# Optimization experiments

Measured on AMD Instinct MI355X. Metric: run time of the kernel, lower is better.

## Reference

```python
import jax, jax.numpy as jnp
import numpy as np

BN_EPS = 1e-5


def grid_sample_bilinear(img, grid):
    """Torch F.grid_sample, mode=bilinear, padding_mode=zeros, align_corners=False.
    img: (B, C, H, W); grid: (B, N, 2) in [-1, 1] -> (B, C, N)."""
    B, C, H, W = img.shape
    x = ((grid[..., 0] + 1.0) * W - 1.0) * 0.5  # (B, N) pixel coords
    y = ((grid[..., 1] + 1.0) * H - 1.0) * 0.5
    x0 = jnp.floor(x)
    y0 = jnp.floor(y)
    x1 = x0 + 1.0
    y1 = y0 + 1.0
    wx1 = x - x0
    wx0 = 1.0 - wx1
    wy1 = y - y0
    wy0 = 1.0 - wy1
    img_flat = img.reshape(B, C, H * W)

    def corner(xi, yi, w):
        valid = (xi >= 0) & (xi <= W - 1) & (yi >= 0) & (yi <= H - 1)
        xi_c = jnp.clip(xi, 0, W - 1).astype(jnp.int32)
        yi_c = jnp.clip(yi, 0, H - 1).astype(jnp.int32)
        idx = yi_c * W + xi_c  # (B, N)
        vals = jnp.take_along_axis(img_flat, idx[:, None, :], axis=2)  # (B, C, N)
        return vals * (w * valid.astype(img.dtype))[:, None, :]

    return (corner(x0, y0, wx0 * wy0) + corner(x1, y0, wx1 * wy0)
            + corner(x0, y1, wx0 * wy1) + corner(x1, y1, wx1 * wy1))


def conv1x1(x, w, b):
    # x: (B, Cin, N), w: (Cout, Cin), b: (Cout,)
    return jnp.einsum('oi,bin->bon', w, x) + b[None, :, None]


def batchnorm1d_train(x, gamma, beta):
    # training-mode BN over (batch, length) per channel, biased variance
    mean = jnp.mean(x, axis=(0, 2), keepdims=True)
    var = jnp.mean((x - mean) ** 2, axis=(0, 2), keepdims=True)
    xn = (x - mean) * jax.lax.rsqrt(var + BN_EPS)
    return xn * gamma[None, :, None] + beta[None, :, None]


def setup_inputs() -> dict:
    key = jax.random.key(0)
    ks = jax.random.split(key, 12)
    B, N, CI, CP, H, W, R = 4, 16384, 256, 256, 64, 160, 4
    Cin = CI + CP
    Cb = CP // R

    def glorot(k, shape):
        fan_in = shape[1]
        return jax.random.normal(k, shape, dtype=jnp.float32) * (1.0 / np.sqrt(fan_in))

    return {
        'pts_img': jax.random.uniform(ks[0], (B, N, 2), dtype=jnp.float32, minval=-1.0, maxval=1.0),
        'img_feats': jax.random.normal(ks[1], (B, CI, H, W), dtype=jnp.float32),
        'pts_feats': jax.random.normal(ks[2], (B, CP, N), dtype=jnp.float32),
        'fusion_w': glorot(ks[3], (CP, Cin)),
        'fusion_b': jax.random.normal(ks[4], (CP,), dtype=jnp.float32) * 0.01,
        'bn_gamma': jnp.ones((CP,), dtype=jnp.float32),
        'bn_beta': jnp.zeros((CP,), dtype=jnp.float32),
        'ca1_w': glorot(ks[5], (Cb, CP)),
        'ca1_b': jax.random.normal(ks[6], (Cb,), dtype=jnp.float32) * 0.01,
        'ca2_w': glorot(ks[7], (CP, Cb)),
        'ca2_b': jax.random.normal(ks[8], (CP,), dtype=jnp.float32) * 0.01,
        'sa_w': glorot(ks[9], (Cb, CP)),
        'sa_b': jax.random.normal(ks[10], (Cb,), dtype=jnp.float32) * 0.01,
    }


def reference(pts_img, img_feats, pts_feats, fusion_w, fusion_b, bn_gamma, bn_beta,
              ca1_w, ca1_b, ca2_w, ca2_b, sa_w, sa_b):
    # grid_sample gather: (B, C_I, N)
    pts_wise_img_feats = grid_sample_bilinear(img_feats, pts_img)
    fusion = jnp.concatenate([pts_wise_img_feats, pts_feats], axis=1)  # (B, C_I+C_P, N)
    # fusion MLP: conv1x1 + BN + ReLU
    fusion = jax.nn.relu(batchnorm1d_train(conv1x1(fusion, fusion_w, fusion_b), bn_gamma, bn_beta))
    # spatial attention: max over channels of bottleneck conv, sigmoid gate
    spatial = jax.nn.sigmoid(jnp.max(conv1x1(fusion, sa_w, sa_b), axis=1, keepdims=True))
    fusion = spatial * fusion
    # channel attention: bottleneck MLP, global max-pool over points, sigmoid gate
    ca = conv1x1(jax.nn.relu(conv1x1(fusion, ca1_w, ca1_b)), ca2_w, ca2_b)  # (B, C_P, N)
    channel = jax.nn.sigmoid(jnp.max(ca, axis=2, keepdims=True))  # (B, C_P, 1)
    return channel * fusion
```

## Files before the change

### kernel.cpp

```cpp
#include <hip/hip_runtime.h>
#include <stdint.h>


typedef __attribute__((ext_vector_type(8))) short bf16x8;
typedef __attribute__((ext_vector_type(4))) float f32x4;

#define B_ 4
#define N_ 16384
#define H_ 64
#define W_ 160
#define HW_ (H_ * W_)
#define K_ 512

__device__ __forceinline__ float bf2f(unsigned short u) {
    union { unsigned int i; float f; } c; c.i = ((unsigned int)u) << 16; return c.f;
}
__device__ __forceinline__ unsigned short f2bf(float f) {
    union { float f; unsigned int i; } c; c.f = f;
    unsigned int u = c.i;
    return (unsigned short)((u + 0x7FFFu + ((u >> 16) & 1u)) >> 16);
}
__device__ __forceinline__ unsigned int fkey(float f) {
    union { float f; unsigned int u; int i; } c; c.f = f;
    return (c.i < 0) ? ~c.u : (c.u | 0x80000000u);
}
__device__ __forceinline__ float funkey(unsigned int k) {
    union { unsigned int u; float f; } c;
    c.u = (k & 0x80000000u) ? (k & 0x7FFFFFFFu) : ~k;
    return c.f;
}

__device__ __forceinline__ void async_copy16(void* lds, const void* g) {
#if defined(__has_builtin) && __has_builtin(__builtin_amdgcn_global_load_lds)
    __builtin_amdgcn_global_load_lds(
        (const __attribute__((address_space(1))) unsigned int*)g,
        (__attribute__((address_space(3))) unsigned int*)lds, 16, 0, 0);
#else
    *(uint4*)lds = *(const uint4*)g;
#endif
}

__global__ __launch_bounds__(256) void k_imgt(const float* __restrict__ img,
                                              unsigned short* __restrict__ imgT,
                                              const float* __restrict__ fw,
                                              const float* __restrict__ saw,
                                              const float* __restrict__ c1w,
                                              const float* __restrict__ c2w,
                                              unsigned short* WfB, unsigned short* saB,
                                              unsigned short* ca1B, unsigned short* ca2B,
                                              float* buckets, unsigned int* camax) {
    int t = threadIdx.x;
    int bx = blockIdx.x;
    if (bx < 2560) {
        __shared__ __align__(16) unsigned short tile[64 * 68];
        int hw0 = (bx % 160) * 64, c0 = ((bx / 160) & 3) * 64, b = bx / 640;
        const float* src = img + ((size_t)b * 256 + c0) * HW_ + hw0;
        int sub = (t & 15) * 4, grp = t >> 4;
#pragma unroll
        for (int it = 0; it < 4; ++it) {
            int cl = grp + it * 16;
            float4 v = *(const float4*)(src + (size_t)cl * HW_ + sub);
            ushort4 o;
            o.x = f2bf(v.x); o.y = f2bf(v.y); o.z = f2bf(v.z); o.w = f2bf(v.w);
            *(ushort4*)(tile + cl * 68 + sub) = o;
        }
        __syncthreads();
        unsigned short* dst = imgT + ((size_t)b * HW_ + hw0) * 256 + c0;
#pragma unroll
        for (int it = 0; it < 4; ++it) {
            int hwl = grp + it * 16;
            ushort4 o;
            o.x = tile[(sub + 0) * 68 + hwl];
            o.y = tile[(sub + 1) * 68 + hwl];
            o.z = tile[(sub + 2) * 68 + hwl];
            o.w = tile[(sub + 3) * 68 + hwl];
            *(ushort4*)(dst + (size_t)hwl * 256 + sub) = o;
        }
    } else {
        int j = bx - 2560;
        if (j == 0) {
            for (int i = t; i < 16 * 512; i += 256) buckets[i] = 0.f;
            for (int i = t; i < 8 * 1024; i += 256) camax[i] = 0u;
        }
        int i = j * 256 + t;
        if (i < 131072) WfB[i] = f2bf(fw[i]);
        else if (i < 147456) saB[i - 131072] = f2bf(saw[i - 131072]);
        else if (i < 163840) ca1B[i - 147456] = f2bf(c1w[i - 147456]);
        else if (i < 180224) ca2B[i - 163840] = f2bf(c2w[i - 163840]);
    }
}

__global__ __launch_bounds__(256, 2) void k_gemm1f(const unsigned short* __restrict__ WfB,
                                                   const float* __restrict__ pim,
                                                   const unsigned short* __restrict__ imgT,
                                                   const float* __restrict__ pts,
                                                   const float* __restrict__ fb,
                                                   unsigned short* __restrict__ Y,
                                                   float* __restrict__ buckets) {
    __shared__ __align__(16) char smem[37888];
    unsigned short* At = (unsigned short*)smem;
    unsigned short* Bt = (unsigned short*)(smem + 16384);
    uint4*  offs4 = (uint4*)(smem + 26624);
    float4* wts4  = (float4*)(smem + 28672);
    unsigned short* tile = (unsigned short*)smem;
    float* biasS = (float*)(smem + 34816);
    float* redS  = (float*)(smem + 35840);
    float* redQ  = (float*)(smem + 36864);

    int t = threadIdx.x;
    int n0 = blockIdx.x * 128, bb = blockIdx.y;
    int w = t >> 6, lane = t & 63, quad = lane >> 4, l15 = lane & 15;
    const unsigned short* imb = imgT + (size_t)bb * HW_ * 256;

    if (t < 128) {
        float2 g2 = *(const float2*)(pim + (size_t)((size_t)bb * N_ + n0 + t) * 2);
        float x = (g2.x + 1.0f) * (0.5f * W_) - 0.5f;
        float y = (g2.y + 1.0f) * (0.5f * H_) - 0.5f;
        float xf = floorf(x), yf = floorf(y);
        float wx1 = x - xf, wx0 = 1.0f - wx1;
        float wy1 = y - yf, wy0 = 1.0f - wy1;
        int x0 = (int)xf, y0 = (int)yf;
        int x1 = x0 + 1, y1 = y0 + 1;
        float vx0 = (x0 >= 0 && x0 < W_) ? 1.f : 0.f;
        float vx1 = (x1 >= 0 && x1 < W_) ? 1.f : 0.f;
        float vy0 = (y0 >= 0 && y0 < H_) ? 1.f : 0.f;
        float vy1 = (y1 >= 0 && y1 < H_) ? 1.f : 0.f;
        int cx0 = min(max(x0, 0), W_ - 1), cx1 = min(max(x1, 0), W_ - 1);
        int cy0 = min(max(y0, 0), H_ - 1), cy1 = min(max(y1, 0), H_ - 1);
        uint4 o4;
        o4.x = (unsigned)(cy0 * W_ + cx0);
        o4.y = (unsigned)(cy0 * W_ + cx1);
        o4.z = (unsigned)(cy1 * W_ + cx0);
        o4.w = (unsigned)(cy1 * W_ + cx1);
        offs4[t] = o4;
        float4 w4;
        w4.x = wx0 * wy0 * vx0 * vy0;
        w4.y = wx1 * wy0 * vx1 * vy0;
        w4.z = wx0 * wy1 * vx0 * vy1;
        w4.w = wx1 * wy1 * vx1 * vy1;
        wts4[t] = w4;
    }

    const f32x4 fzero = {0.f, 0.f, 0.f, 0.f};
    f32x4 acc[4][8];
#pragma unroll
    for (int i = 0; i < 4; ++i)
#pragma unroll
        for (int j = 0; j < 8; ++j) acc[i][j] = fzero;

    for (int kt = 0; kt < 16; ++kt) {
        int k0 = kt * 32;
        __syncthreads();
#pragma unroll
        for (int q = 0; q < 4; ++q) {
            int row = q * 64 + (t >> 2);
            async_copy16(At + (size_t)q * 2048 + (size_t)t * 8,
                         WfB + (size_t)row * K_ + k0 + (t & 3) * 8);
        }
        if (kt < 8) {
#pragma unroll
            for (int pass = 0; pass < 2; ++pass) {
                int tau = pass * 256 + t;
                int pt = tau >> 2, cg = tau & 3;
                uint4 o4 = offs4[pt];
                float4 w4 = wts4[pt];
                int ch = k0 + cg * 8;
                uint4 cA = *(const uint4*)(imb + (size_t)o4.x * 256 + ch);
                uint4 cB = *(const uint4*)(imb + (size_t)o4.y * 256 + ch);
                uint4 cC = *(const uint4*)(imb + (size_t)o4.z * 256 + ch);
                uint4 cD = *(const uint4*)(imb + (size_t)o4.w * 256 + ch);
                const unsigned short* pa = (const unsigned short*)&cA;
                const unsigned short* pb = (const unsigned short*)&cB;
                const unsigned short* pc = (const unsigned short*)&cC;
                const unsigned short* pd = (const unsigned short*)&cD;
                uint4 ov;
                unsigned short* po = (unsigned short*)&ov;
#pragma unroll
                for (int e = 0; e < 8; ++e)
                    po[e] = f2bf(w4.x * bf2f(pa[e]) + w4.y * bf2f(pb[e]) +
                                 w4.z * bf2f(pc[e]) + w4.w * bf2f(pd[e]));
                *(uint4*)(Bt + pt * 40 + cg * 8) = ov;
            }
        } else {
            int c_local = t & 31, g = t >> 5;
            int c = (kt - 8) * 32 + c_local;
            const float* src = pts + ((size_t)bb * 256 + c) * (size_t)N_ + n0 + g * 16;
            float4 v0 = *(const float4*)(src + 0);
            float4 v1 = *(const float4*)(src + 4);
            float4 v2 = *(const float4*)(src + 8);
            float4 v3 = *(const float4*)(src + 12);
            unsigned short* dst = Bt + (size_t)g * 16 * 40 + c_local;
            dst[0 * 40] = f2bf(v0.x); dst[1 * 40] = f2bf(v0.y);
            dst[2 * 40] = f2bf(v0.z); dst[3 * 40] = f2bf(v0.w);
            dst[4 * 40] = f2bf(v1.x); dst[5 * 40] = f2bf(v1.y);
            dst[6 * 40] = f2bf(v1.z); dst[7 * 40] = f2bf(v1.w);
            dst[8 * 40] = f2bf(v2.x); dst[9 * 40] = f2bf(v2.y);
            dst[10 * 40] = f2bf(v2.z); dst[11 * 40] = f2bf(v2.w);
            dst[12 * 40] = f2bf(v3.x); dst[13 * 40] = f2bf(v3.y);
            dst[14 * 40] = f2bf(v3.z); dst[15 * 40] = f2bf(v3.w);
        }
        __syncthreads();
        bf16x8 af[4], bv[8];
#pragma unroll
        for (int j = 0; j < 8; ++j)
            bv[j] = *(const bf16x8*)(Bt + (j * 16 + l15) * 40 + quad * 8);
#pragma unroll
        for (int i = 0; i < 4; ++i)
            af[i] = *(const bf16x8*)(At + (w * 64 + i * 16 + l15) * 32 + quad * 8);
#pragma unroll
        for (int i = 0; i < 4; ++i)
#pragma unroll
            for (int j = 0; j < 8; ++j)
                acc[i][j] = __builtin_amdgcn_mfma_f32_16x16x32_bf16(af[i], bv[j], acc[i][j], 0, 0, 0);
    }

    __syncthreads();
    biasS[t] = fb[t];
    __syncthreads();
#pragma unroll
    for (int i = 0; i < 4; ++i) {
        int mq = w * 64 + i * 16 + quad * 4;
#pragma unroll
        for (int r = 0; r < 4; ++r) {
            float bia = biasS[mq + r];
            float s = 0.f, q = 0.f;
#pragma unroll
            for (int j = 0; j < 8; ++j) {
                float y = acc[i][j][r] + bia;
                s += y; q += y * y;
            }
#pragma unroll
            for (int d = 1; d < 16; d <<= 1) {
                s += __shfl_xor(s, d, 64);
                q += __shfl_xor(q, d, 64);
            }
            if (l15 == 0) { redS[mq + r] = s; redQ[mq + r] = q; }
        }
    }
    size_t Yrow0 = ((size_t)bb * N_ + n0) * 256;
#pragma unroll
    for (int h = 0; h < 2; ++h) {
        if (h == 1) __syncthreads();
        if ((w >> 1) == h) {
            int hw = w & 1;
#pragma unroll
            for (int i = 0; i < 4; ++i) {
                int mloc = hw * 64 + i * 16 + quad * 4;
                int mg = h * 128 + mloc;
                float b0 = biasS[mg + 0], b1 = biasS[mg + 1];
                float b2 = biasS[mg + 2], b3 = biasS[mg + 3];
#pragma unroll
                for (int j = 0; j < 8; ++j) {
                    int n = j * 16 + l15;
                    ushort4 o;
                    o.x = f2bf(acc[i][j][0] + b0);
                    o.y = f2bf(acc[i][j][1] + b1);
                    o.z = f2bf(acc[i][j][2] + b2);
                    o.w = f2bf(acc[i][j][3] + b3);
                    *(ushort4*)(tile + n * 136 + mloc) = o;
                }
            }
        }
        __syncthreads();
        if (h == 0) {
            float* bk = buckets + (size_t)(blockIdx.x & 15) * 512;
            atomicAdd(bk + t, redS[t]);
            atomicAdd(bk + 256 + t, redQ[t]);
        }
#pragma unroll
        for (int pass = 0; pass < 8; ++pass) {
            int row = pass * 16 + (t >> 4);
            int cB = (t & 15) * 8;
            uint4 v = *(const uint4*)(tile + row * 136 + cB);
            *(uint4*)(Y + Yrow0 + (size_t)row * 256 + h * 128 + cB) = v;
        }
    }
}

__global__ __launch_bounds__(256, 2) void k_gate(const unsigned short* __restrict__ Y,
                                                 const float* __restrict__ buckets,
                                                 const float* __restrict__ gamma,
                                                 const float* __restrict__ beta,
                                                 const unsigned short* __restrict__ saB,
                                                 const float* __restrict__ sab,
                                                 const unsigned short* __restrict__ c1B,
                                                 const float* __restrict__ c1b,
                                                 const unsigned short* __restrict__ c2B,
                                                 unsigned int* __restrict__ camax,
                                                 float* __restrict__ sp_g,
                                                 float* __restrict__ ss_out) {
    __shared__ __align__(16) unsigned short Ft[64 * 264];
    __shared__ __align__(16) unsigned short Ht[64 * 72];
    __shared__ float scS[256], shS[256];
    __shared__ float saPart[4][64];
    __shared__ float spL[64];
    int t = threadIdx.x;
    size_t pts0 = (size_t)blockIdx.x * 64;
    int b = (int)(pts0 >> 14);
    int w = t >> 6, lane = t & 63, quad = lane >> 4, l15 = lane & 15;
    int jrow = w * 16 + l15;

    bf16x8 bvs[8], bvc[8];
#pragma unroll
    for (int kt = 0; kt < 8; ++kt) {
        bvs[kt] = *(const bf16x8*)(saB + (size_t)jrow * 256 + kt * 32 + quad * 8);
        bvc[kt] = *(const bf16x8*)(c1B + (size_t)jrow * 256 + kt * 32 + quad * 8);
    }
    float sbias = sab[jrow];
    float cbias = c1b[jrow];

    {
        float s = 0.f, q = 0.f;
#pragma unroll
        for (int bk = 0; bk < 16; ++bk) {
            s += buckets[bk * 512 + t];
            q += buckets[bk * 512 + 256 + t];
        }
        const float inv = 1.0f / (float)(B_ * N_);
        float mean = s * inv;
        float var = q * inv - mean * mean;
        float sc = gamma[t] * rsqrtf(var + 1e-5f);
        float sh = beta[t] - mean * sc;
        scS[t] = sc;
        shS[t] = sh;
        if (blockIdx.x == 0) { ss_out[t] = sc; ss_out[256 + t] = sh; }
    }
    __syncthreads();

    int cc = (t * 8) & 255;
    float scr[8], shr[8];
#pragma unroll
    for (int e = 0; e < 8; ++e) { scr[e] = scS[cc + e]; shr[e] = shS[cc + e]; }
    for (int idx = t * 8; idx < 64 * 256; idx += 2048) {
        int r = idx >> 8;
        uint4 v = *(const uint4*)(Y + (pts0 + r) * 256 + cc);
        unsigned short* us = (unsigned short*)&v;
#pragma unroll
        for (int e = 0; e < 8; ++e) {
            float f = bf2f(us[e]) * scr[e] + shr[e];
            us[e] = f2bf(fmaxf(f, 0.f));
        }
        *(uint4*)(Ft + r * 264 + cc) = v;
    }
    __syncthreads();

    const f32x4 fzero = {0.f, 0.f, 0.f, 0.f};
    f32x4 accS[4], accC[4];
#pragma unroll
    for (int i = 0; i < 4; ++i) { accS[i] = fzero; accC[i] = fzero; }
#pragma unroll
    for (int kt = 0; kt < 8; ++kt) {
        bf16x8 af[4];
#pragma unroll
        for (int i = 0; i < 4; ++i)
            af[i] = *(const bf16x8*)(Ft + (i * 16 + l15) * 264 + kt * 32 + quad * 8);
#pragma unroll
        for (int i = 0; i < 4; ++i) {
            accS[i] = __builtin_amdgcn_mfma_f32_16x16x32_bf16(af[i], bvs[kt], accS[i], 0, 0, 0);
            accC[i] = __builtin_amdgcn_mfma_f32_16x16x32_bf16(af[i], bvc[kt], accC[i], 0, 0, 0);
        }
    }
#pragma unroll
    for (int i = 0; i < 4; ++i) {
#pragma unroll
        for (int r = 0; r < 4; ++r) {
            float v = accS[i][r] + sbias;
#pragma unroll
            for (int d = 1; d < 16; d <<= 1) v = fmaxf(v, __shfl_xor(v, d, 64));
            if (l15 == 0) saPart[w][i * 16 + quad * 4 + r] = v;
        }
    }
    __syncthreads();
    if (t < 64) {
        float m4 = fmaxf(fmaxf(saPart[0][t], saPart[1][t]),
                         fmaxf(saPart[2][t], saPart[3][t]));
        float sv = 1.0f / (1.0f + __expf(-m4));
        spL[t] = sv;
        sp_g[pts0 + t] = sv;
    }
    __syncthreads();

#pragma unroll
    for (int i = 0; i < 4; ++i) {
#pragma unroll
        for (int r = 0; r < 4; ++r) {
            int pt = i * 16 + quad * 4 + r;
            float hv = fmaxf(accC[i][r] * spL[pt] + cbias, 0.f);
            Ht[pt * 72 + jrow] = f2bf(hv);
        }
    }
    __syncthreads();

    {
        bf16x8 b2a[4], b2b[4];
#pragma unroll
        for (int mt = 0; mt < 4; ++mt) {
            b2a[mt] = *(const bf16x8*)(c2B + (size_t)(w * 64 + mt * 16 + l15) * 64 + quad * 8);
            b2b[mt] = *(const bf16x8*)(c2B + (size_t)(w * 64 + mt * 16 + l15) * 64 + 32 + quad * 8);
        }
        float vmax[4] = {-3e38f, -3e38f, -3e38f, -3e38f};
#pragma unroll
        for (int i = 0; i < 4; ++i) {
            bf16x8 a0 = *(const bf16x8*)(Ht + (i * 16 + l15) * 72 + quad * 8);
            bf16x8 a1 = *(const bf16x8*)(Ht + (i * 16 + l15) * 72 + 32 + quad * 8);
#pragma unroll
            for (int mt = 0; mt < 4; ++mt) {
                f32x4 acc = __builtin_amdgcn_mfma_f32_16x16x32_bf16(a0, b2a[mt], fzero, 0, 0, 0);
                acc = __builtin_amdgcn_mfma_f32_16x16x32_bf16(a1, b2b[mt], acc, 0, 0, 0);
#pragma unroll
                for (int r = 0; r < 4; ++r) vmax[mt] = fmaxf(vmax[mt], acc[r]);
            }
        }
        unsigned int* cam = camax + (size_t)(blockIdx.x & 7) * 1024 + b * 256;
#pragma unroll
        for (int mt = 0; mt < 4; ++mt) {
            float v = vmax[mt];
            v = fmaxf(v, __shfl_xor(v, 16, 64));
            v = fmaxf(v, __shfl_xor(v, 32, 64));
            if (quad == 0) atomicMax(cam + w * 64 + mt * 16 + l15, fkey(v));
        }
    }
}

__global__ __launch_bounds__(256) void k_out(const unsigned short* __restrict__ Y,
                                             const unsigned int* __restrict__ camax,
                                             const float* __restrict__ c2b,
                                             const float* __restrict__ ss,
                                             const float* __restrict__ sp_g,
                                             float* __restrict__ out) {
    __shared__ __align__(16) unsigned short tile[64 * 68];
    __shared__ float ch[64], scT[64], shT[64], spT[64];
    int t = threadIdx.x;
    int n0 = blockIdx.x * 64, m0 = blockIdx.y * 64, b = blockIdx.z;
    if (t < 64) {
        int m = m0 + t;
        unsigned int k = 0u;
#pragma unroll
        for (int bk = 0; bk < 8; ++bk) k = max(k, camax[bk * 1024 + b * 256 + m]);
        ch[t] = 1.0f / (1.0f + __expf(-(funkey(k) + c2b[m])));
        scT[t] = ss[m];
        shT[t] = ss[256 + m];
        spT[t] = sp_g[(size_t)b * N_ + n0 + t];
    }
    int sub = (t & 15) * 4, grp = t >> 4;
    const unsigned short* src = Y + ((size_t)b * N_ + n0) * 256 + m0;
#pragma unroll
    for (int it = 0; it < 4; ++it) {
        int nl = grp + it * 16;
        ushort4 v = *(const ushort4*)(src + (size_t)nl * 256 + sub);
        *(ushort4*)(tile + nl * 68 + sub) = v;
    }
    __syncthreads();
    float* dst = out + ((size_t)b * 256 + m0) * N_ + n0;
#pragma unroll
    for (int it = 0; it < 4; ++it) {
        int ml = grp + it * 16;
        float g = ch[ml], scv = scT[ml], shv = shT[ml];
        float4 o;
        o.x = fmaxf(bf2f(tile[(sub + 0) * 68 + ml]) * scv + shv, 0.f) * spT[sub + 0] * g;
        o.y = fmaxf(bf2f(tile[(sub + 1) * 68 + ml]) * scv + shv, 0.f) * spT[sub + 1] * g;
        o.z = fmaxf(bf2f(tile[(sub + 2) * 68 + ml]) * scv + shv, 0.f) * spT[sub + 2] * g;
        o.w = fmaxf(bf2f(tile[(sub + 3) * 68 + ml]) * scv + shv, 0.f) * spT[sub + 3] * g;
        *(float4*)(dst + (size_t)ml * N_ + sub) = o;
    }
}

extern "C" void kernel_launch(void* const* d_in, const int* in_sizes, int n_in,
                              void* d_out, int out_size, void* d_ws, size_t ws_size,
                              hipStream_t stream) {
    (void)in_sizes; (void)n_in; (void)out_size; (void)ws_size;
    const float* pts_img = (const float*)d_in[0];
    const float* img     = (const float*)d_in[1];
    const float* pts     = (const float*)d_in[2];
    const float* fw      = (const float*)d_in[3];
    const float* fbias   = (const float*)d_in[4];
    const float* gamma   = (const float*)d_in[5];
    const float* beta    = (const float*)d_in[6];
    const float* c1w     = (const float*)d_in[7];
    const float* c1b     = (const float*)d_in[8];
    const float* c2w     = (const float*)d_in[9];
    const float* c2b     = (const float*)d_in[10];
    const float* saw     = (const float*)d_in[11];
    const float* sab     = (const float*)d_in[12];
    float* out = (float*)d_out;

    char* ws = (char*)d_ws;
    unsigned short* imgT = (unsigned short*)(ws);
    unsigned short* Y    = (unsigned short*)(ws + 20971520);
    unsigned short* WfB  = (unsigned short*)(ws + 54525952);
    unsigned short* saB  = (unsigned short*)(ws + 54788096);
    unsigned short* ca1B = (unsigned short*)(ws + 54820864);
    unsigned short* ca2B = (unsigned short*)(ws + 54853632);
    float* buckets       = (float*)(ws + 54886400);
    unsigned int* camax  = (unsigned int*)(ws + 54919168);
    float* sp_g          = (float*)(ws + 54951936);
    float* ss            = (float*)(ws + 55214080);

    k_imgt<<<3264, 256, 0, stream>>>(img, imgT, fw, saw, c1w, c2w,
                                     WfB, saB, ca1B, ca2B, buckets, camax);
    k_gemm1f<<<dim3(128, 4), 256, 0, stream>>>(WfB, pts_img, imgT, pts, fbias, Y, buckets);
    k_gate<<<1024, 256, 0, stream>>>(Y, buckets, gamma, beta, saB, sab, ca1B, c1b,
                                     ca2B, camax, sp_g, ss);
    k_out<<<dim3(256, 4, 4), 256, 0, stream>>>(Y, camax, c2b, ss, sp_g, out);
}
```

Baseline: 247.3 us.

## Apply fusion weights to image grid before sampling, then bilinearly gather projected features

The first conv is linear and bilinear sampling is linear, so the image half of the fusion weight is now applied to the full image grid (4x10240 pixels) in a new GEMM kernel. The main GEMM only handles the point-feature half of K and then gathers and interpolates the projected 256-channel features, adding them in the epilogue. This removes the separate image transpose pass and halves the main GEMM's K. In exchange it does a GEMM over 40960 pixels instead of 65536 points, and rounding differs because the projected features are stored in bf16 before interpolation.

Result: slower. 280.5 us (+13.4%).

```diff
diff --git a/kernel.cpp b/kernel.cpp
--- a/kernel.cpp
+++ b/kernel.cpp
@@ -40,9 +40,7 @@
 #endif
 }
 
-__global__ __launch_bounds__(256) void k_imgt(const float* __restrict__ img,
-                                              unsigned short* __restrict__ imgT,
-                                              const float* __restrict__ fw,
+__global__ __launch_bounds__(256) void k_init(const float* __restrict__ fw,
                                               const float* __restrict__ saw,
                                               const float* __restrict__ c1w,
                                               const float* __restrict__ c2w,
@@ -50,67 +48,110 @@
                                               unsigned short* ca1B, unsigned short* ca2B,
                                               float* buckets, unsigned int* camax) {
     int t = threadIdx.x;
-    int bx = blockIdx.x;
-    if (bx < 2560) {
-        __shared__ __align__(16) unsigned short tile[64 * 68];
-        int hw0 = (bx % 160) * 64, c0 = ((bx / 160) & 3) * 64, b = bx / 640;
-        const float* src = img + ((size_t)b * 256 + c0) * HW_ + hw0;
-        int sub = (t & 15) * 4, grp = t >> 4;
-#pragma unroll
-        for (int it = 0; it < 4; ++it) {
-            int cl = grp + it * 16;
-            float4 v = *(const float4*)(src + (size_t)cl * HW_ + sub);
+    int j = blockIdx.x;
+    if (j == 0) {
+        for (int i = t; i < 16 * 512; i += 256) buckets[i] = 0.f;
+        for (int i = t; i < 8 * 1024; i += 256) camax[i] = 0u;
+    }
+    int i = j * 256 + t;
+    if (i < 131072) WfB[i] = f2bf(fw[i]);
+    else if (i < 147456) saB[i - 131072] = f2bf(saw[i - 131072]);
+    else if (i < 163840) ca1B[i - 147456] = f2bf(c1w[i - 147456]);
+    else if (i < 180224) ca2B[i - 163840] = f2bf(c2w[i - 163840]);
+}
+
+__global__ __launch_bounds__(256, 3) void k_zimg(const unsigned short* __restrict__ WfB,
+                                                 const float* __restrict__ img,
+                                                 unsigned short* __restrict__ ZT) {
+    __shared__ __align__(16) char smem[21504];
+    unsigned short* At = (unsigned short*)smem;
+    unsigned short* Bt = (unsigned short*)(smem + 16384);
+
+    int t = threadIdx.x;
+    int hw0 = blockIdx.x * 64, b = blockIdx.y;
+    int w = t >> 6, lane = t & 63, quad = lane >> 4, l15 = lane & 15;
+
+    const f32x4 fzero = {0.f, 0.f, 0.f, 0.f};
+    f32x4 acc[4][4];
+#pragma unroll
+    for (int i = 0; i < 4; ++i)
+#pragma unroll
+        for (int j = 0; j < 4; ++j) acc[i][j] = fzero;
+
+    for (int kt = 0; kt < 8; ++kt) {
+        int k0 = kt * 32;
+        __syncthreads();
+#pragma unroll
+        for (int q = 0; q < 4; ++q) {
+            int row = q * 64 + (t >> 2);
+            async_copy16(At + (size_t)q * 2048 + (size_t)t * 8,
+                         WfB + (size_t)row * K_ + k0 + (t & 3) * 8);
+        }
+        {
+            int c_local = t & 31, g = t >> 5;
+            int c = k0 + c_local;
+            const float* src = img + ((size_t)b * 256 + c) * (size_t)HW_ + hw0 + g * 8;
+            float4 v0 = *(const float4*)(src + 0);
+            float4 v1 = *(const float4*)(src + 4);
+            unsigned short* dst = Bt + (size_t)(g * 8) * 40 + c_local;
+            dst[0 * 40] = f2bf(v0.x); dst[1 * 40] = f2bf(v0.y);
+            dst[2 * 40] = f2bf(v0.z); dst[3 * 40] = f2bf(v0.w);
+            dst[4 * 40] = f2bf(v1.x); dst[5 * 40] = f2bf(v1.y);
+            dst[6 * 40] = f2bf(v1.z); dst[7 * 40] = f2bf(v1.w);
+        }
+        __syncthreads();
+        bf16x8 af[4], bv[4];
+#pragma unroll
+        for (int j = 0; j < 4; ++j)
+            bv[j] = *(const bf16x8*)(Bt + (j * 16 + l15) * 40 + quad * 8);
+#pragma unroll
+        for (int i = 0; i < 4; ++i)
+            af[i] = *(const bf16x8*)(At + (w * 64 + i * 16 + l15) * 32 + quad * 8);
+#pragma unroll
+        for (int i = 0; i < 4; ++i)
+#pragma unroll
+            for (int j = 0; j < 4; ++j)
+                acc[i][j] = __builtin_amdgcn_mfma_f32_16x16x32_bf16(af[i], bv[j], acc[i][j], 0, 0, 0);
+    }
+
+    unsigned short* Zb = ZT + ((size_t)b * HW_ + hw0) * 256;
+#pragma unroll
+    for (int i = 0; i < 4; ++i) {
+        int m = w * 64 + i * 16 + quad * 4;
+#pragma unroll
+        for (int j = 0; j < 4; ++j) {
+            int n = j * 16 + l15;
             ushort4 o;
-            o.x = f2bf(v.x); o.y = f2bf(v.y); o.z = f2bf(v.z); o.w = f2bf(v.w);
-            *(ushort4*)(tile + cl * 68 + sub) = o;
-        }
-        __syncthreads();
-        unsigned short* dst = imgT + ((size_t)b * HW_ + hw0) * 256 + c0;
-#pragma unroll
-        for (int it = 0; it < 4; ++it) {
-            int hwl = grp + it * 16;
-            ushort4 o;
-            o.x = tile[(sub + 0) * 68 + hwl];
-            o.y = tile[(sub + 1) * 68 + hwl];
-            o.z = tile[(sub + 2) * 68 + hwl];
-            o.w = tile[(sub + 3) * 68 + hwl];
-            *(ushort4*)(dst + (size_t)hwl * 256 + sub) = o;
-        }
-    } else {
-        int j = bx - 2560;
-        if (j == 0) {
-            for (int i = t; i < 16 * 512; i += 256) buckets[i] = 0.f;
-            for (int i = t; i < 8 * 1024; i += 256) camax[i] = 0u;
-        }
-        int i = j * 256 + t;
-        if (i < 131072) WfB[i] = f2bf(fw[i]);
-        else if (i < 147456) saB[i - 131072] = f2bf(saw[i - 131072]);
-        else if (i < 163840) ca1B[i - 147456] = f2bf(c1w[i - 147456]);
-        else if (i < 180224) ca2B[i - 163840] = f2bf(c2w[i - 163840]);
-    }
-}
-
-__global__ __launch_bounds__(256, 2) void k_gemm1f(const unsigned short* __restrict__ WfB,
+            o.x = f2bf(acc[i][j][0]);
+            o.y = f2bf(acc[i][j][1]);
+            o.z = f2bf(acc[i][j][2]);
+            o.w = f2bf(acc[i][j][3]);
+            *(ushort4*)(Zb + (size_t)n * 256 + m) = o;
+        }
+    }
+}
+
+__global__ __launch_bounds__(256, 2) void k_gemm1p(const unsigned short* __restrict__ WfB,
                                                    const float* __restrict__ pim,
-                                                   const unsigned short* __restrict__ imgT,
+                                                   const unsigned short* __restrict__ ZT,
                                                    const float* __restrict__ pts,
                                                    const float* __restrict__ fb,
                                                    unsigned short* __restrict__ Y,
                                                    float* __restrict__ buckets) {
-    __shared__ __align__(16) char smem[37888];
+    __shared__ __align__(16) char smem[41984];
     unsigned short* At = (unsigned short*)smem;
     unsigned short* Bt = (unsigned short*)(smem + 16384);
-    uint4*  offs4 = (uint4*)(smem + 26624);
-    float4* wts4  = (float4*)(smem + 28672);
     unsigned short* tile = (unsigned short*)smem;
     float* biasS = (float*)(smem + 34816);
     float* redS  = (float*)(smem + 35840);
     float* redQ  = (float*)(smem + 36864);
+    uint4*  offs4 = (uint4*)(smem + 37888);
+    float4* wts4  = (float4*)(smem + 39936);
 
     int t = threadIdx.x;
     int n0 = blockIdx.x * 128, bb = blockIdx.y;
     int w = t >> 6, lane = t & 63, quad = lane >> 4, l15 = lane & 15;
-    const unsigned short* imb = imgT + (size_t)bb * HW_ * 256;
+    const unsigned short* Zb = ZT + (size_t)bb * HW_ * 256;
 
     if (t < 128) {
         float2 g2 = *(const float2*)(pim + (size_t)((size_t)bb * N_ + n0 + t) * 2);
@@ -140,6 +181,7 @@
         w4.w = wx1 * wy1 * vx1 * vy1;
         wts4[t] = w4;
     }
+    biasS[t] = fb[t];
 
     const f32x4 fzero = {0.f, 0.f, 0.f, 0.f};
     f32x4 acc[4][8];
@@ -148,42 +190,18 @@
 #pragma unroll
         for (int j = 0; j < 8; ++j) acc[i][j] = fzero;
 
-    for (int kt = 0; kt < 16; ++kt) {
+    for (int kt = 0; kt < 8; ++kt) {
         int k0 = kt * 32;
         __syncthreads();
 #pragma unroll
         for (int q = 0; q < 4; ++q) {
             int row = q * 64 + (t >> 2);
             async_copy16(At + (size_t)q * 2048 + (size_t)t * 8,
-                         WfB + (size_t)row * K_ + k0 + (t & 3) * 8);
-        }
-        if (kt < 8) {
-#pragma unroll
-            for (int pass = 0; pass < 2; ++pass) {
-                int tau = pass * 256 + t;
-                int pt = tau >> 2, cg = tau & 3;
-                uint4 o4 = offs4[pt];
-                float4 w4 = wts4[pt];
-                int ch = k0 + cg * 8;
-                uint4 cA = *(const uint4*)(imb + (size_t)o4.x * 256 + ch);
-                uint4 cB = *(const uint4*)(imb + (size_t)o4.y * 256 + ch);
-                uint4 cC = *(const uint4*)(imb + (size_t)o4.z * 256 + ch);
-                uint4 cD = *(const uint4*)(imb + (size_t)o4.w * 256 + ch);
-                const unsigned short* pa = (const unsigned short*)&cA;
-                const unsigned short* pb = (const unsigned short*)&cB;
-                const unsigned short* pc = (const unsigned short*)&cC;
-                const unsigned short* pd = (const unsigned short*)&cD;
-                uint4 ov;
-                unsigned short* po = (unsigned short*)&ov;
-#pragma unroll
-                for (int e = 0; e < 8; ++e)
-                    po[e] = f2bf(w4.x * bf2f(pa[e]) + w4.y * bf2f(pb[e]) +
-                                 w4.z * bf2f(pc[e]) + w4.w * bf2f(pd[e]));
-                *(uint4*)(Bt + pt * 40 + cg * 8) = ov;
-            }
-        } else {
+                         WfB + (size_t)row * K_ + 256 + k0 + (t & 3) * 8);
+        }
+        {
             int c_local = t & 31, g = t >> 5;
-            int c = (kt - 8) * 32 + c_local;
+            int c = k0 + c_local;
             const float* src = pts + ((size_t)bb * 256 + c) * (size_t)N_ + n0 + g * 16;
             float4 v0 = *(const float4*)(src + 0);
             float4 v1 = *(const float4*)(src + 4);
@@ -215,32 +233,42 @@
     }
 
     __syncthreads();
-    biasS[t] = fb[t];
-    __syncthreads();
-#pragma unroll
-    for (int i = 0; i < 4; ++i) {
-        int mq = w * 64 + i * 16 + quad * 4;
-#pragma unroll
-        for (int r = 0; r < 4; ++r) {
-            float bia = biasS[mq + r];
-            float s = 0.f, q = 0.f;
-#pragma unroll
-            for (int j = 0; j < 8; ++j) {
-                float y = acc[i][j][r] + bia;
-                s += y; q += y * y;
-            }
-#pragma unroll
-            for (int d = 1; d < 16; d <<= 1) {
-                s += __shfl_xor(s, d, 64);
-                q += __shfl_xor(q, d, 64);
-            }
-            if (l15 == 0) { redS[mq + r] = s; redQ[mq + r] = q; }
-        }
-    }
+
     size_t Yrow0 = ((size_t)bb * N_ + n0) * 256;
 #pragma unroll
     for (int h = 0; h < 2; ++h) {
         if (h == 1) __syncthreads();
+        {
+            int pt = t >> 1;
+            uint4 o4 = offs4[pt];
+            float4 w4 = wts4[pt];
+            const unsigned short* pA = Zb + (size_t)o4.x * 256;
+            const unsigned short* pB = Zb + (size_t)o4.y * 256;
+            const unsigned short* pC = Zb + (size_t)o4.z * 256;
+            const unsigned short* pD = Zb + (size_t)o4.w * 256;
+            int mbase = h * 128 + (t & 1) * 64;
+            int lbase = (t & 1) * 64;
+#pragma unroll
+            for (int s = 0; s < 8; ++s) {
+                int mc = mbase + s * 8;
+                uint4 cA = *(const uint4*)(pA + mc);
+                uint4 cB = *(const uint4*)(pB + mc);
+                uint4 cC = *(const uint4*)(pC + mc);
+                uint4 cD = *(const uint4*)(pD + mc);
+                const unsigned short* qa = (const unsigned short*)&cA;
+                const unsigned short* qb = (const unsigned short*)&cB;
+                const unsigned short* qc = (const unsigned short*)&cC;
+                const unsigned short* qd = (const unsigned short*)&cD;
+                uint4 ov;
+                unsigned short* po = (unsigned short*)&ov;
+#pragma unroll
+                for (int e = 0; e < 8; ++e)
+                    po[e] = f2bf(w4.x * bf2f(qa[e]) + w4.y * bf2f(qb[e]) +
+                                 w4.z * bf2f(qc[e]) + w4.w * bf2f(qd[e]));
+                *(uint4*)(tile + pt * 136 + lbase + s * 8) = ov;
+            }
+        }
+        __syncthreads();
         if ((w >> 1) == h) {
             int hw = w & 1;
 #pragma unroll
@@ -249,30 +277,51 @@
                 int mg = h * 128 + mloc;
                 float b0 = biasS[mg + 0], b1 = biasS[mg + 1];
                 float b2 = biasS[mg + 2], b3 = biasS[mg + 3];
+                float s0 = 0.f, q0 = 0.f, s1 = 0.f, q1 = 0.f;
+                float s2 = 0.f, q2 = 0.f, s3 = 0.f, q3 = 0.f;
 #pragma unroll
                 for (int j = 0; j < 8; ++j) {
                     int n = j * 16 + l15;
+                    ushort4 v = *(const ushort4*)(tile + n * 136 + mloc);
+                    float y0 = acc[i][j][0] + bf2f(v.x) + b0;
+                    float y1 = acc[i][j][1] + bf2f(v.y) + b1;
+                    float y2 = acc[i][j][2] + bf2f(v.z) + b2;
+                    float y3 = acc[i][j][3] + bf2f(v.w) + b3;
+                    s0 += y0; q0 += y0 * y0;
+                    s1 += y1; q1 += y1 * y1;
+                    s2 += y2; q2 += y2 * y2;
+                    s3 += y3; q3 += y3 * y3;
                     ushort4 o;
-                    o.x = f2bf(acc[i][j][0] + b0);
-                    o.y = f2bf(acc[i][j][1] + b1);
-                    o.z = f2bf(acc[i][j][2] + b2);
-                    o.w = f2bf(acc[i][j][3] + b3);
+                    o.x = f2bf(y0); o.y = f2bf(y1); o.z = f2bf(y2); o.w = f2bf(y3);
                     *(ushort4*)(tile + n * 136 + mloc) = o;
                 }
+#pragma unroll
+                for (int d = 1; d < 16; d <<= 1) {
+                    s0 += __shfl_xor(s0, d, 64); q0 += __shfl_xor(q0, d, 64);
+                    s1 += __shfl_xor(s1, d, 64); q1 += __shfl_xor(q1, d, 64);
+                    s2 += __shfl_xor(s2, d, 64); q2 += __shfl_xor(q2, d, 64);
+                    s3 += __shfl_xor(s3, d, 64); q3 += __shfl_xor(q3, d, 64);
+                }
+                if (l15 == 0) {
+                    redS[mg + 0] = s0; redQ[mg + 0] = q0;
+                    redS[mg + 1] = s1; redQ[mg + 1] = q1;
+                    redS[mg + 2] = s2; redQ[mg + 2] = q2;
+                    redS[mg + 3] = s3; redQ[mg + 3] = q3;
+                }
             }
         }
         __syncthreads();
-        if (h == 0) {
+        if (t < 128) {
             float* bk = buckets + (size_t)(blockIdx.x & 15) * 512;
-            atomicAdd(bk + t, redS[t]);
-            atomicAdd(bk + 256 + t, redQ[t]);
+            atomicAdd(bk + h * 128 + t, redS[h * 128 + t]);
+            atomicAdd(bk + 256 + h * 128 + t, redQ[h * 128 + t]);
         }
 #pragma unroll
         for (int pass = 0; pass < 8; ++pass) {
             int row = pass * 16 + (t >> 4);
-            int cB = (t & 15) * 8;
-            uint4 v = *(const uint4*)(tile + row * 136 + cB);
-            *(uint4*)(Y + Yrow0 + (size_t)row * 256 + h * 128 + cB) = v;
+            int cB2 = (t & 15) * 8;
+            uint4 v = *(const uint4*)(tile + row * 136 + cB2);
+            *(uint4*)(Y + Yrow0 + (size_t)row * 256 + h * 128 + cB2) = v;
         }
     }
 }
@@ -485,7 +534,7 @@
     float* out = (float*)d_out;
 
     char* ws = (char*)d_ws;
-    unsigned short* imgT = (unsigned short*)(ws);
+    unsigned short* ZT   = (unsigned short*)(ws);
     unsigned short* Y    = (unsigned short*)(ws + 20971520);
     unsigned short* WfB  = (unsigned short*)(ws + 54525952);
     unsigned short* saB  = (unsigned short*)(ws + 54788096);
@@ -496,9 +545,9 @@
     float* sp_g          = (float*)(ws + 54951936);
     float* ss            = (float*)(ws + 55214080);
 
-    k_imgt<<<3264, 256, 0, stream>>>(img, imgT, fw, saw, c1w, c2w,
-                                     WfB, saB, ca1B, ca2B, buckets, camax);
-    k_gemm1f<<<dim3(128, 4), 256, 0, stream>>>(WfB, pts_img, imgT, pts, fbias, Y, buckets);
+    k_init<<<704, 256, 0, stream>>>(fw, saw, c1w, c2w, WfB, saB, ca1B, ca2B, buckets, camax);
+    k_zimg<<<dim3(160, 4), 256, 0, stream>>>(WfB, img, ZT);
+    k_gemm1p<<<dim3(128, 4), 256, 0, stream>>>(WfB, pts_img, ZT, pts, fbias, Y, buckets);
     k_gate<<<1024, 256, 0, stream>>>(Y, buckets, gamma, beta, saB, sab, ca1B, c1b,
                                      ca2B, camax, sp_g, ss);
     k_out<<<dim3(256, 4, 4), 256, 0, stream>>>(Y, camax, c2b, ss, sp_g, out);
```

## Halve GEMM1 point tile to 64 and raise occupancy to four blocks per CU

Applied to the files above, without the earlier changes.

The fused gather+GEMM kernel now handles 64 points per block instead of 128. This halves the accumulator registers, doubles the grid to 1024 blocks, and lets launch bounds request 4 blocks per CU. The epilogue is restructured to write the full 256-channel tile to shared memory in one pass, fusing the BN statistics reduction with the bf16 store, and the bias load is hoisted before the K loop. The weight tile is now reloaded twice as often per point, and 16 atomics per bucket slot double in count, in exchange for better latency hiding of the bilinear gathers.

Result: no change. 248.4 us (+0.5%).

```diff
diff --git a/kernel.cpp b/kernel.cpp
--- a/kernel.cpp
+++ b/kernel.cpp
@@ -90,29 +90,29 @@
     }
 }
 
-__global__ __launch_bounds__(256, 2) void k_gemm1f(const unsigned short* __restrict__ WfB,
+__global__ __launch_bounds__(256, 4) void k_gemm1f(const unsigned short* __restrict__ WfB,
                                                    const float* __restrict__ pim,
                                                    const unsigned short* __restrict__ imgT,
                                                    const float* __restrict__ pts,
                                                    const float* __restrict__ fb,
                                                    unsigned short* __restrict__ Y,
                                                    float* __restrict__ buckets) {
-    __shared__ __align__(16) char smem[37888];
+    __shared__ __align__(16) char smem[38912];
     unsigned short* At = (unsigned short*)smem;
     unsigned short* Bt = (unsigned short*)(smem + 16384);
-    uint4*  offs4 = (uint4*)(smem + 26624);
-    float4* wts4  = (float4*)(smem + 28672);
     unsigned short* tile = (unsigned short*)smem;
-    float* biasS = (float*)(smem + 34816);
-    float* redS  = (float*)(smem + 35840);
-    float* redQ  = (float*)(smem + 36864);
+    uint4*  offs4 = (uint4*)(smem + 33792);
+    float4* wts4  = (float4*)(smem + 34816);
+    float* biasS = (float*)(smem + 35840);
+    float* redS  = (float*)(smem + 36864);
+    float* redQ  = (float*)(smem + 37888);
 
     int t = threadIdx.x;
-    int n0 = blockIdx.x * 128, bb = blockIdx.y;
+    int n0 = blockIdx.x * 64, bb = blockIdx.y;
     int w = t >> 6, lane = t & 63, quad = lane >> 4, l15 = lane & 15;
     const unsigned short* imb = imgT + (size_t)bb * HW_ * 256;
 
-    if (t < 128) {
+    if (t < 64) {
         float2 g2 = *(const float2*)(pim + (size_t)((size_t)bb * N_ + n0 + t) * 2);
         float x = (g2.x + 1.0f) * (0.5f * W_) - 0.5f;
         float y = (g2.y + 1.0f) * (0.5f * H_) - 0.5f;
@@ -140,13 +140,14 @@
         w4.w = wx1 * wy1 * vx1 * vy1;
         wts4[t] = w4;
     }
+    biasS[t] = fb[t];
 
     const f32x4 fzero = {0.f, 0.f, 0.f, 0.f};
-    f32x4 acc[4][8];
+    f32x4 acc[4][4];
 #pragma unroll
     for (int i = 0; i < 4; ++i)
 #pragma unroll
-        for (int j = 0; j < 8; ++j) acc[i][j] = fzero;
+        for (int j = 0; j < 4; ++j) acc[i][j] = fzero;
 
     for (int kt = 0; kt < 16; ++kt) {
         int k0 = kt * 32;
@@ -158,51 +159,41 @@
                          WfB + (size_t)row * K_ + k0 + (t & 3) * 8);
         }
         if (kt < 8) {
-#pragma unroll
-            for (int pass = 0; pass < 2; ++pass) {
-                int tau = pass * 256 + t;
-                int pt = tau >> 2, cg = tau & 3;
-                uint4 o4 = offs4[pt];
-                float4 w4 = wts4[pt];
-                int ch = k0 + cg * 8;
-                uint4 cA = *(const uint4*)(imb + (size_t)o4.x * 256 + ch);
-                uint4 cB = *(const uint4*)(imb + (size_t)o4.y * 256 + ch);
-                uint4 cC = *(const uint4*)(imb + (size_t)o4.z * 256 + ch);
-                uint4 cD = *(const uint4*)(imb + (size_t)o4.w * 256 + ch);
-                const unsigned short* pa = (const unsigned short*)&cA;
-                const unsigned short* pb = (const unsigned short*)&cB;
-                const unsigned short* pc = (const unsigned short*)&cC;
-                const unsigned short* pd = (const unsigned short*)&cD;
-                uint4 ov;
-                unsigned short* po = (unsigned short*)&ov;
-#pragma unroll
-                for (int e = 0; e < 8; ++e)
-                    po[e] = f2bf(w4.x * bf2f(pa[e]) + w4.y * bf2f(pb[e]) +
-                                 w4.z * bf2f(pc[e]) + w4.w * bf2f(pd[e]));
-                *(uint4*)(Bt + pt * 40 + cg * 8) = ov;
-            }
+            int pt = t >> 2, cg = t & 3;
+            uint4 o4 = offs4[pt];
+            float4 w4 = wts4[pt];
+            int ch = k0 + cg * 8;
+            uint4 cA = *(const uint4*)(imb + (size_t)o4.x * 256 + ch);
+            uint4 cB = *(const uint4*)(imb + (size_t)o4.y * 256 + ch);
+            uint4 cC = *(const uint4*)(imb + (size_t)o4.z * 256 + ch);
+            uint4 cD = *(const uint4*)(imb + (size_t)o4.w * 256 + ch);
+            const unsigned short* pa = (const unsigned short*)&cA;
+            const unsigned short* pb = (const unsigned short*)&cB;
+            const unsigned short* pc = (const unsigned short*)&cC;
+            const unsigned short* pd = (const unsigned short*)&cD;
+            uint4 ov;
+            unsigned short* po = (unsigned short*)&ov;
+#pragma unroll
+            for (int e = 0; e < 8; ++e)
+                po[e] = f2bf(w4.x * bf2f(pa[e]) + w4.y * bf2f(pb[e]) +
+                             w4.z * bf2f(pc[e]) + w4.w * bf2f(pd[e]));
+            *(uint4*)(Bt + pt * 40 + cg * 8) = ov;
         } else {
             int c_local = t & 31, g = t >> 5;
             int c = (kt - 8) * 32 + c_local;
-            const float* src = pts + ((size_t)bb * 256 + c) * (size_t)N_ + n0 + g * 16;
+            const float* src = pts + ((size_t)bb * 256 + c) * (size_t)N_ + n0 + g * 8;
             float4 v0 = *(const float4*)(src + 0);
             float4 v1 = *(const float4*)(src + 4);
-            float4 v2 = *(const float4*)(src + 8);
-            float4 v3 = *(const float4*)(src + 12);
-            unsigned short* dst = Bt + (size_t)g * 16 * 40 + c_local;
+            unsigned short* dst = Bt + (size_t)(g * 8) * 40 + c_local;
             dst[0 * 40] = f2bf(v0.x); dst[1 * 40] = f2bf(v0.y);
             dst[2 * 40] = f2bf(v0.z); dst[3 * 40] = f2bf(v0.w);
             dst[4 * 40] = f2bf(v1.x); dst[5 * 40] = f2bf(v1.y);
             dst[6 * 40] = f2bf(v1.z); dst[7 * 40] = f2bf(v1.w);
-            dst[8 * 40] = f2bf(v2.x); dst[9 * 40] = f2bf(v2.y);
-            dst[10 * 40] = f2bf(v2.z); dst[11 * 40] = f2bf(v2.w);
-            dst[12 * 40] = f2bf(v3.x); dst[13 * 40] = f2bf(v3.y);
-            dst[14 * 40] = f2bf(v3.z); dst[15 * 40] = f2bf(v3.w);
         }
         __syncthreads();
-        bf16x8 af[4], bv[8];
-#pragma unroll
-        for (int j = 0; j < 8; ++j)
+        bf16x8 af[4], bv[4];
+#pragma unroll
+        for (int j = 0; j < 4; ++j)
             bv[j] = *(const bf16x8*)(Bt + (j * 16 + l15) * 40 + quad * 8);
 #pragma unroll
         for (int i = 0; i < 4; ++i)
@@ -210,70 +201,59 @@
 #pragma unroll
         for (int i = 0; i < 4; ++i)
 #pragma unroll
-            for (int j = 0; j < 8; ++j)
+            for (int j = 0; j < 4; ++j)
                 acc[i][j] = __builtin_amdgcn_mfma_f32_16x16x32_bf16(af[i], bv[j], acc[i][j], 0, 0, 0);
     }
 
     __syncthreads();
-    biasS[t] = fb[t];
-    __syncthreads();
 #pragma unroll
     for (int i = 0; i < 4; ++i) {
-        int mq = w * 64 + i * 16 + quad * 4;
-#pragma unroll
-        for (int r = 0; r < 4; ++r) {
-            float bia = biasS[mq + r];
-            float s = 0.f, q = 0.f;
-#pragma unroll
-            for (int j = 0; j < 8; ++j) {
-                float y = acc[i][j][r] + bia;
-                s += y; q += y * y;
-            }
-#pragma unroll
-            for (int d = 1; d < 16; d <<= 1) {
-                s += __shfl_xor(s, d, 64);
-                q += __shfl_xor(q, d, 64);
-            }
-            if (l15 == 0) { redS[mq + r] = s; redQ[mq + r] = q; }
-        }
+        int mloc = w * 64 + i * 16 + quad * 4;
+        float b0 = biasS[mloc + 0], b1 = biasS[mloc + 1];
+        float b2 = biasS[mloc + 2], b3 = biasS[mloc + 3];
+        float s0 = 0.f, q0 = 0.f, s1 = 0.f, q1 = 0.f;
+        float s2 = 0.f, q2 = 0.f, s3 = 0.f, q3 = 0.f;
+#pragma unroll
+        for (int j = 0; j < 4; ++j) {
+            int n = j * 16 + l15;
+            float y0 = acc[i][j][0] + b0;
+            float y1 = acc[i][j][1] + b1;
+            float y2 = acc[i][j][2] + b2;
+            float y3 = acc[i][j][3] + b3;
+            s0 += y0; q0 += y0 * y0;
+            s1 += y1; q1 += y1 * y1;
+            s2 += y2; q2 += y2 * y2;
+            s3 += y3; q3 += y3 * y3;
+            ushort4 o;
+            o.x = f2bf(y0); o.y = f2bf(y1); o.z = f2bf(y2); o.w = f2bf(y3);
+            *(ushort4*)(tile + n * 264 + mloc) = o;
+        }
+#pragma unroll
+        for (int d = 1; d < 16; d <<= 1) {
+            s0 += __shfl_xor(s0, d, 64); q0 += __shfl_xor(q0, d, 64);
+            s1 += __shfl_xor(s1, d, 64); q1 += __shfl_xor(q1, d, 64);
+            s2 += __shfl_xor(s2, d, 64); q2 += __shfl_xor(q2, d, 64);
+            s3 += __shfl_xor(s3, d, 64); q3 += __shfl_xor(q3, d, 64);
+        }
+        if (l15 == 0) {
+            redS[mloc + 0] = s0; redQ[mloc + 0] = q0;
+            redS[mloc + 1] = s1; redQ[mloc + 1] = q1;
+            redS[mloc + 2] = s2; redQ[mloc + 2] = q2;
+            redS[mloc + 3] = s3; redQ[mloc + 3] = q3;
+        }
+    }
+    __syncthreads();
+    {
+        float* bk = buckets + (size_t)(blockIdx.x & 15) * 512;
+        atomicAdd(bk + t, redS[t]);
+        atomicAdd(bk + 256 + t, redQ[t]);
     }
     size_t Yrow0 = ((size_t)bb * N_ + n0) * 256;
 #pragma unroll
-    for (int h = 0; h < 2; ++h) {
-        if (h == 1) __syncthreads();
-        if ((w >> 1) == h) {
-            int hw = w & 1;
-#pragma unroll
-            for (int i = 0; i < 4; ++i) {
-                int mloc = hw * 64 + i * 16 + quad * 4;
-                int mg = h * 128 + mloc;
-                float b0 = biasS[mg + 0], b1 = biasS[mg + 1];
-                float b2 = biasS[mg + 2], b3 = biasS[mg + 3];
-#pragma unroll
-                for (int j = 0; j < 8; ++j) {
-                    int n = j * 16 + l15;
-                    ushort4 o;
-                    o.x = f2bf(acc[i][j][0] + b0);
-                    o.y = f2bf(acc[i][j][1] + b1);
-                    o.z = f2bf(acc[i][j][2] + b2);
-                    o.w = f2bf(acc[i][j][3] + b3);
-                    *(ushort4*)(tile + n * 136 + mloc) = o;
-                }
-            }
-        }
-        __syncthreads();
-        if (h == 0) {
-            float* bk = buckets + (size_t)(blockIdx.x & 15) * 512;
-            atomicAdd(bk + t, redS[t]);
-            atomicAdd(bk + 256 + t, redQ[t]);
-        }
-#pragma unroll
-        for (int pass = 0; pass < 8; ++pass) {
-            int row = pass * 16 + (t >> 4);
-            int cB = (t & 15) * 8;
-            uint4 v = *(const uint4*)(tile + row * 136 + cB);
-            *(uint4*)(Y + Yrow0 + (size_t)row * 256 + h * 128 + cB) = v;
-        }
+    for (int pass = 0; pass < 8; ++pass) {
+        int row = pass * 8 + (t >> 5);
+        int col = (t & 31) * 8;
+        *(uint4*)(Y + Yrow0 + (size_t)row * 256 + col) = *(const uint4*)(tile + row * 264 + col);
     }
 }
 
@@ -498,7 +478,7 @@
 
     k_imgt<<<3264, 256, 0, stream>>>(img, imgT, fw, saw, c1w, c2w,
                                      WfB, saB, ca1B, ca2B, buckets, camax);
-    k_gemm1f<<<dim3(128, 4), 256, 0, stream>>>(WfB, pts_img, imgT, pts, fbias, Y, buckets);
+    k_gemm1f<<<dim3(256, 4), 256, 0, stream>>>(WfB, pts_img, imgT, pts, fbias, Y, buckets);
     k_gate<<<1024, 256, 0, stream>>>(Y, buckets, gamma, beta, saB, sab, ca1B, c1b,
                                      ca2B, camax, sp_g, ss);
     k_out<<<dim3(256, 4, 4), 256, 0, stream>>>(Y, camax, c2b, ss, sp_g, out);
```
